# Kernel optimization log

Measured on AMD Instinct MI355X. Metric: run time of the kernel, lower is better.

The kernel has to match this reference:

```python
import jax, jax.numpy as jnp
import numpy as np

N_NODES = 50000
N_EDGES = 800000
D_IN = 128
D_OUT = 128


def setup_inputs() -> dict:
    key = jax.random.key(0)
    k1, k2, k3, k4, k5, k6 = jax.random.split(key, 6)
    x = jax.random.normal(k1, (N_NODES, D_IN), dtype=jnp.float32)
    edge_row = jnp.sort(jax.random.randint(k2, (N_EDGES,), 0, N_NODES, dtype=jnp.int32))
    edge_col = jax.random.randint(k3, (N_EDGES,), 0, N_NODES, dtype=jnp.int32)
    edge_val = jax.random.uniform(k4, (N_EDGES,), dtype=jnp.float32)
    W = jax.random.uniform(k5, (D_OUT, D_IN), dtype=jnp.float32)  # torch Linear weight [out,in], uniform_ init
    b = jax.random.normal(k6, (D_OUT,), dtype=jnp.float32)
    return {"x": x, "edge_row": edge_row, "edge_col": edge_col,
            "edge_val": edge_val, "W": W, "b": b}


def reference(x, edge_row, edge_col, edge_val, W, b):
    # spmm: out[i] = sum_{e: row[e]==i} val[e] * x[col[e]]
    msgs = x[edge_col] * edge_val[:, None]            # [E, D_IN]
    agg = jax.ops.segment_sum(msgs, edge_row, num_segments=x.shape[0])  # [N, D_IN]
    # dropout is identity in eval mode; linear projection y = agg @ W^T + b
    return agg @ W.T + b
```

## Files before the change

### kernel.cpp

```cpp
#include <hip/hip_runtime.h>
#include <hip/hip_bf16.h>


#define NPB     16
#define BLOCK   256
#define D       128
#define CHUNK   512
#define ASTRIDE 136

typedef __attribute__((ext_vector_type(8))) short bf16x8;
typedef __attribute__((ext_vector_type(4))) float f32x4;

__device__ __forceinline__ short f2bf(float f) {
    unsigned u = __float_as_uint(f);
    unsigned r = (u + 0x7fffu + ((u >> 16) & 1u)) >> 16;
    return (short)r;
}
__device__ __forceinline__ float bf_lo(int w) { return __int_as_float(w << 16); }
__device__ __forceinline__ float bf_hi(int w) { return __int_as_float(w & 0xffff0000); }

__global__ __launch_bounds__(256)
void prepass_kernel(const float* __restrict__ x,
                    const float* __restrict__ W,
                    const int*   __restrict__ edge_row,
                    short* __restrict__ xb,
                    short* __restrict__ wb,
                    int*   __restrict__ rs,
                    int n_nodes, int n_edges, int n4, int nw4)
{
    const int gid = blockIdx.x * 256 + threadIdx.x;

    if (gid <= n_nodes) {
        int lo = 0, hi = n_edges;
        while (lo < hi) {
            int mid = (lo + hi) >> 1;
            bool lt = (edge_row[mid] < gid);
            lo = lt ? (mid + 1) : lo;
            hi = lt ? hi : mid;
        }
        rs[gid] = lo;
    }

    const int i = gid - (n_nodes + 1);
    if (i >= 0 && i < n4) {
        float4 v = reinterpret_cast<const float4*>(x)[i];
        reinterpret_cast<short4*>(xb)[i] =
            make_short4(f2bf(v.x), f2bf(v.y), f2bf(v.z), f2bf(v.w));
    }

    const int iw = i - n4;
    if (iw >= 0 && iw < nw4) {
        float4 v = reinterpret_cast<const float4*>(W)[iw];
        reinterpret_cast<short4*>(wb)[iw] =
            make_short4(f2bf(v.x), f2bf(v.y), f2bf(v.z), f2bf(v.w));
    }
}

__global__ __launch_bounds__(BLOCK, 8)
void gcn_main_kernel(const short* __restrict__ xb,
                     const short* __restrict__ wb,
                     const int*   __restrict__ rs_g,
                     const int*   __restrict__ edge_col,
                     const float* __restrict__ edge_val,
                     const float* __restrict__ bvec,
                     float*       __restrict__ out,
                     int n_nodes, int n_edges)
{
    __shared__ int2  cv_s[CHUNK];
    __shared__ __align__(16) short agg_s[NPB * ASTRIDE];
    __shared__ int rs_s[NPB + 1];

    const int tid  = threadIdx.x;
    const int wave = tid >> 6;
    const int lane = tid & 63;
    const int tile_base = blockIdx.x * NPB;

    if (tid <= NPB) rs_s[tid] = rs_g[tile_base + tid];
    __syncthreads();

    const int E0 = __builtin_amdgcn_readfirstlane(rs_s[0]);
    const int E1 = __builtin_amdgcn_readfirstlane(rs_s[NPB]);

    const int p = lane >> 4;
    const int q = lane & 15;
    const int n = wave * 4 + p;
    const int e0 = rs_s[n], e1 = rs_s[n + 1];
    const short* xq = xb + q * 8;

    float2 acc2[4];
    #pragma unroll
    for (int i = 0; i < 4; ++i) acc2[i] = make_float2(0.f, 0.f);

    for (int cb = E0; cb < E1; cb += CHUNK) {
        const int cnt = min(E1 - cb, CHUNK);
        __syncthreads();
        for (int i = tid; i < cnt; i += BLOCK) {
            cv_s[i] = make_int2(edge_col[cb + i], __float_as_int(edge_val[cb + i]));
        }
        __syncthreads();

        const int s = max(e0, cb);
        const int t = min(e1, cb + cnt);
        int m = t - s;
        int mm = max(m, __shfl_xor(m, 16, 64));
        mm = max(mm, __shfl_xor(mm, 32, 64));
        mm = __builtin_amdgcn_readfirstlane(mm);

        for (int it = 0; it < mm; it += 8) {
            #pragma unroll
            for (int u = 0; u < 8; ++u) {
                int idx = s + it + u;
                bool ok = (idx < t);
                int il = ok ? (idx - cb) : 0;
                int2 cv = cv_s[il];
                float v = ok ? __int_as_float(cv.y) : 0.f;
                int4 xr = *reinterpret_cast<const int4*>(xq + ((size_t)cv.x << 7));
                float2 p0 = make_float2(bf_lo(xr.x), bf_hi(xr.x));
                float2 p1 = make_float2(bf_lo(xr.y), bf_hi(xr.y));
                float2 p2 = make_float2(bf_lo(xr.z), bf_hi(xr.z));
                float2 p3 = make_float2(bf_lo(xr.w), bf_hi(xr.w));
                acc2[0].x = fmaf(v, p0.x, acc2[0].x); acc2[0].y = fmaf(v, p0.y, acc2[0].y);
                acc2[1].x = fmaf(v, p1.x, acc2[1].x); acc2[1].y = fmaf(v, p1.y, acc2[1].y);
                acc2[2].x = fmaf(v, p2.x, acc2[2].x); acc2[2].y = fmaf(v, p2.y, acc2[2].y);
                acc2[3].x = fmaf(v, p3.x, acc2[3].x); acc2[3].y = fmaf(v, p3.y, acc2[3].y);
            }
        }
    }

    {
        bf16x8 o;
        o[0] = f2bf(acc2[0].x); o[1] = f2bf(acc2[0].y);
        o[2] = f2bf(acc2[1].x); o[3] = f2bf(acc2[1].y);
        o[4] = f2bf(acc2[2].x); o[5] = f2bf(acc2[2].y);
        o[6] = f2bf(acc2[3].x); o[7] = f2bf(acc2[3].y);
        *reinterpret_cast<bf16x8*>(&agg_s[n * ASTRIDE + q * 8]) = o;
    }

    const int n16 = lane & 15;
    const int g   = lane >> 4;

    bf16x8 bfr[2][4];
    float  bj[2];
    #pragma unroll
    for (int tt = 0; tt < 2; ++tt) {
        const int jt = 2 * wave + tt;
        const short* wrow = wb + ((size_t)(jt * 16 + n16)) * D + g * 8;
        #pragma unroll
        for (int ks = 0; ks < 4; ++ks) {
            bfr[tt][ks] = *reinterpret_cast<const bf16x8*>(wrow + ks * 32);
        }
        bj[tt] = bvec[jt * 16 + n16];
    }

    __syncthreads();

    {
        bf16x8 afr[4];
        #pragma unroll
        for (int ks = 0; ks < 4; ++ks) {
            afr[ks] = *reinterpret_cast<const bf16x8*>(
                &agg_s[n16 * ASTRIDE + ks * 32 + g * 8]);
        }

        #pragma unroll
        for (int tt = 0; tt < 2; ++tt) {
            const int jt = 2 * wave + tt;
            const int j  = jt * 16 + n16;

            f32x4 c = {0.f, 0.f, 0.f, 0.f};
            #pragma unroll
            for (int ks = 0; ks < 4; ++ks) {
                c = __builtin_amdgcn_mfma_f32_16x16x32_bf16(afr[ks], bfr[tt][ks], c, 0, 0, 0);
            }
            #pragma unroll
            for (int r = 0; r < 4; ++r) {
                int node = tile_base + g * 4 + r;
                if (node < n_nodes)
                    out[(size_t)node * D + j] = c[r] + bj[tt];
            }
        }
    }
}

__global__ __launch_bounds__(BLOCK, 5)
void gcn_fallback_kernel(const float* __restrict__ x,
                         const int*   __restrict__ edge_row,
                         const int*   __restrict__ edge_col,
                         const float* __restrict__ edge_val,
                         const float* __restrict__ W,
                         const float* __restrict__ bvec,
                         float*       __restrict__ out,
                         int n_nodes, int n_edges)
{
    __shared__ __align__(16) short agg_s[NPB * ASTRIDE];
    __shared__ int rs_s[NPB + 1];

    const int tid  = threadIdx.x;
    const int wave = tid >> 6;
    const int lane = tid & 63;
    const int tile_base = blockIdx.x * NPB;

    if (tid <= NPB) {
        int target = tile_base + tid;
        if (target > n_nodes) target = n_nodes;
        int lo = 0, hi = n_edges;
        while (lo < hi) {
            int mid = (lo + hi) >> 1;
            lo = (edge_row[mid] < target) ? (mid + 1) : lo;
            hi = (edge_row[mid] < target) ? hi : mid;
        }
        rs_s[tid] = lo;
    }
    __syncthreads();

    {
        const int h = lane >> 5;
        const int q = lane & 31;
        const float* xq = x + (q << 2);

        #pragma unroll
        for (int ni = 0; ni < NPB / 4; ++ni) {
            const int n = wave + 4 * ni;
            const int e0 = __builtin_amdgcn_readfirstlane(rs_s[n]);
            const int e1 = __builtin_amdgcn_readfirstlane(rs_s[n + 1]);
            float ax = 0.f, ay = 0.f, az = 0.f, aw = 0.f;
            for (int e = e0; e < e1; e += 16) {
                #pragma unroll
                for (int u = 0; u < 8; ++u) {
                    int idx  = e + 2 * u + h;
                    int idxc = (idx < e1) ? idx : (e1 - 1);
                    int   c  = edge_col[idxc];
                    float vr = edge_val[idxc];
                    float v  = (idx < e1) ? vr : 0.f;
                    float4 xr = *reinterpret_cast<const float4*>(xq + ((size_t)c << 7));
                    ax += v * xr.x; ay += v * xr.y; az += v * xr.z; aw += v * xr.w;
                }
            }
            ax += __shfl_xor(ax, 32, 64); ay += __shfl_xor(ay, 32, 64);
            az += __shfl_xor(az, 32, 64); aw += __shfl_xor(aw, 32, 64);
            if (h == 0) {
                *reinterpret_cast<short4*>(&agg_s[n * ASTRIDE + (q << 2)]) =
                    make_short4(f2bf(ax), f2bf(ay), f2bf(az), f2bf(aw));
            }
        }
    }

    const int n16 = lane & 15;
    const int g   = lane >> 4;
    bf16x8 bfr[2][4];
    #pragma unroll
    for (int tt = 0; tt < 2; ++tt) {
        const int jt = 2 * wave + tt;
        const float* rowp = W + ((size_t)(jt * 16 + n16)) * D + g * 8;
        #pragma unroll
        for (int ks = 0; ks < 4; ++ks) {
            float4 wa = *reinterpret_cast<const float4*>(rowp + ks * 32);
            float4 wb4 = *reinterpret_cast<const float4*>(rowp + ks * 32 + 4);
            bf16x8 f;
            f[0] = f2bf(wa.x); f[1] = f2bf(wa.y); f[2] = f2bf(wa.z); f[3] = f2bf(wa.w);
            f[4] = f2bf(wb4.x); f[5] = f2bf(wb4.y); f[6] = f2bf(wb4.z); f[7] = f2bf(wb4.w);
            bfr[tt][ks] = f;
        }
    }
    __syncthreads();
    {
        bf16x8 afr[4];
        #pragma unroll
        for (int ks = 0; ks < 4; ++ks)
            afr[ks] = *reinterpret_cast<const bf16x8*>(&agg_s[n16 * ASTRIDE + ks * 32 + g * 8]);
        #pragma unroll
        for (int tt = 0; tt < 2; ++tt) {
            const int jt = 2 * wave + tt;
            const int j  = jt * 16 + n16;
            const float bj = bvec[j];
            f32x4 c = {0.f, 0.f, 0.f, 0.f};
            #pragma unroll
            for (int ks = 0; ks < 4; ++ks)
                c = __builtin_amdgcn_mfma_f32_16x16x32_bf16(afr[ks], bfr[tt][ks], c, 0, 0, 0);
            #pragma unroll
            for (int r = 0; r < 4; ++r) {
                int node = tile_base + g * 4 + r;
                if (node < n_nodes)
                    out[(size_t)node * D + j] = c[r] + bj;
            }
        }
    }
}

extern "C" void kernel_launch(void* const* d_in, const int* in_sizes, int n_in,
                              void* d_out, int out_size, void* d_ws, size_t ws_size,
                              hipStream_t stream) {
    const float* x        = (const float*)d_in[0];
    const int*   edge_row = (const int*)  d_in[1];
    const int*   edge_col = (const int*)  d_in[2];
    const float* edge_val = (const float*)d_in[3];
    const float* W        = (const float*)d_in[4];
    const float* b        = (const float*)d_in[5];
    float* out = (float*)d_out;

    const int n_nodes = in_sizes[0] / D;
    const int n_edges = in_sizes[1];
    const int grid = (n_nodes + NPB - 1) / NPB;

    const size_t xb_bytes = (size_t)n_nodes * D * sizeof(short);
    const size_t rs_bytes = (size_t)(n_nodes + 1) * sizeof(int);
    const size_t wb_bytes = (size_t)D * D * sizeof(short);
    if (ws_size >= xb_bytes + rs_bytes + wb_bytes) {
        short* xb = (short*)d_ws;
        int*   rs = (int*)((char*)d_ws + xb_bytes);
        short* wb = (short*)((char*)d_ws + xb_bytes + rs_bytes);
        const int n4  = n_nodes * D / 4;
        const int nw4 = D * D / 4;
        const int total = (n_nodes + 1) + n4 + nw4;
        prepass_kernel<<<(total + 255) / 256, 256, 0, stream>>>(
            x, W, edge_row, xb, wb, rs, n_nodes, n_edges, n4, nw4);
        gcn_main_kernel<<<grid, BLOCK, 0, stream>>>(xb, wb, rs, edge_col, edge_val,
                                                    b, out, n_nodes, n_edges);
    } else {
        gcn_fallback_kernel<<<grid, BLOCK, 0, stream>>>(x, edge_row, edge_col, edge_val,
                                                        W, b, out, n_nodes, n_edges);
    }
}
```

Before: 127.9 us.

## Stage one edge chunk per block and batch gathers per node with global fallback

Replaces the per-chunk loop with its block-wide barriers by a single staging of up to one chunk of edges into shared memory. Each node group then walks only its own edges, issuing eight gathers before the FMAs so more loads are in flight; edges past the staged chunk are read straight from global memory. Accumulation uses packed two-float vectors, and the occupancy hint drops from 8 to 6 waves per SIMD to allow more registers for the batched loads. The risk is lower occupancy, plus a slow serial global path for the rare blocks with more edges than fit in one chunk.

```diff
diff --git a/kernel.cpp b/kernel.cpp
--- a/kernel.cpp
+++ b/kernel.cpp
@@ -10,6 +10,7 @@
 
 typedef __attribute__((ext_vector_type(8))) short bf16x8;
 typedef __attribute__((ext_vector_type(4))) float f32x4;
+typedef __attribute__((ext_vector_type(2))) float v2f;
 
 __device__ __forceinline__ short f2bf(float f) {
     unsigned u = __float_as_uint(f);
@@ -56,7 +57,7 @@
     }
 }
 
-__global__ __launch_bounds__(BLOCK, 8)
+__global__ __launch_bounds__(BLOCK, 6)
 void gcn_main_kernel(const short* __restrict__ xb,
                      const short* __restrict__ wb,
                      const int*   __restrict__ rs_g,
@@ -80,51 +81,57 @@
 
     const int E0 = __builtin_amdgcn_readfirstlane(rs_s[0]);
     const int E1 = __builtin_amdgcn_readfirstlane(rs_s[NPB]);
+    const int cnt = min(E1 - E0, CHUNK);
+
+    for (int i = tid; i < cnt; i += BLOCK) {
+        cv_s[i] = make_int2(edge_col[E0 + i], __float_as_int(edge_val[E0 + i]));
+    }
+    __syncthreads();
 
     const int p = lane >> 4;
     const int q = lane & 15;
     const int n = wave * 4 + p;
     const int e0 = rs_s[n], e1 = rs_s[n + 1];
+    const int cap  = E0 + cnt;
+    const int ecap = min(e1, cap);
     const short* xq = xb + q * 8;
 
-    float2 acc2[4];
+    v2f acc2[4];
     #pragma unroll
-    for (int i = 0; i < 4; ++i) acc2[i] = make_float2(0.f, 0.f);
-
-    for (int cb = E0; cb < E1; cb += CHUNK) {
-        const int cnt = min(E1 - cb, CHUNK);
-        __syncthreads();
-        for (int i = tid; i < cnt; i += BLOCK) {
-            cv_s[i] = make_int2(edge_col[cb + i], __float_as_int(edge_val[cb + i]));
-        }
-        __syncthreads();
-
-        const int s = max(e0, cb);
-        const int t = min(e1, cb + cnt);
-        int m = t - s;
-        int mm = max(m, __shfl_xor(m, 16, 64));
-        mm = max(mm, __shfl_xor(mm, 32, 64));
-        mm = __builtin_amdgcn_readfirstlane(mm);
-
-        for (int it = 0; it < mm; it += 8) {
-            #pragma unroll
-            for (int u = 0; u < 8; ++u) {
-                int idx = s + it + u;
-                bool ok = (idx < t);
-                int il = ok ? (idx - cb) : 0;
-                int2 cv = cv_s[il];
-                float v = ok ? __int_as_float(cv.y) : 0.f;
-                int4 xr = *reinterpret_cast<const int4*>(xq + ((size_t)cv.x << 7));
-                float2 p0 = make_float2(bf_lo(xr.x), bf_hi(xr.x));
-                float2 p1 = make_float2(bf_lo(xr.y), bf_hi(xr.y));
-                float2 p2 = make_float2(bf_lo(xr.z), bf_hi(xr.z));
-                float2 p3 = make_float2(bf_lo(xr.w), bf_hi(xr.w));
-                acc2[0].x = fmaf(v, p0.x, acc2[0].x); acc2[0].y = fmaf(v, p0.y, acc2[0].y);
-                acc2[1].x = fmaf(v, p1.x, acc2[1].x); acc2[1].y = fmaf(v, p1.y, acc2[1].y);
-                acc2[2].x = fmaf(v, p2.x, acc2[2].x); acc2[2].y = fmaf(v, p2.y, acc2[2].y);
-                acc2[3].x = fmaf(v, p3.x, acc2[3].x); acc2[3].y = fmaf(v, p3.y, acc2[3].y);
-            }
-        }
+    for (int i = 0; i < 4; ++i) acc2[i] = (v2f){0.f, 0.f};
+
+    for (int e = e0; e < ecap; e += 8) {
+        int2  cv[8];
+        int4  xr[8];
+        #pragma unroll
+        for (int u = 0; u < 8; ++u) {
+            int idx = e + u;
+            int il  = (idx < ecap) ? (idx - E0) : (e0 - E0);
+            cv[u] = cv_s[il];
+        }
+        #pragma unroll
+        for (int u = 0; u < 8; ++u) {
+            xr[u] = *reinterpret_cast<const int4*>(xq + ((size_t)cv[u].x << 7));
+        }
+        #pragma unroll
+        for (int u = 0; u < 8; ++u) {
+            float vm = (e + u < ecap) ? __int_as_float(cv[u].y) : 0.f;
+            v2f v2 = (v2f){vm, vm};
+            acc2[0] += v2 * (v2f){bf_lo(xr[u].x), bf_hi(xr[u].x)};
+            acc2[1] += v2 * (v2f){bf_lo(xr[u].y), bf_hi(xr[u].y)};
+            acc2[2] += v2 * (v2f){bf_lo(xr[u].z), bf_hi(xr[u].z)};
+            acc2[3] += v2 * (v2f){bf_lo(xr[u].w), bf_hi(xr[u].w)};
+        }
+    }
+    for (int e = max(e0, cap); e < e1; ++e) {
+        int   c = edge_col[e];
+        float v = edge_val[e];
+        int4 xr = *reinterpret_cast<const int4*>(xq + ((size_t)c << 7));
+        v2f v2 = (v2f){v, v};
+        acc2[0] += v2 * (v2f){bf_lo(xr.x), bf_hi(xr.x)};
+        acc2[1] += v2 * (v2f){bf_lo(xr.y), bf_hi(xr.y)};
+        acc2[2] += v2 * (v2f){bf_lo(xr.z), bf_hi(xr.z)};
+        acc2[3] += v2 * (v2f){bf_lo(xr.w), bf_hi(xr.w)};
     }
 
     {
@@ -254,10 +261,10 @@
         const float* rowp = W + ((size_t)(jt * 16 + n16)) * D + g * 8;
         #pragma unroll
         for (int ks = 0; ks < 4; ++ks) {
-            float4 wa = *reinterpret_cast<const float4*>(rowp + ks * 32);
+            float4 wa  = *reinterpret_cast<const float4*>(rowp + ks * 32);
             float4 wb4 = *reinterpret_cast<const float4*>(rowp + ks * 32 + 4);
             bf16x8 f;
-            f[0] = f2bf(wa.x); f[1] = f2bf(wa.y); f[2] = f2bf(wa.z); f[3] = f2bf(wa.w);
+            f[0] = f2bf(wa.x);  f[1] = f2bf(wa.y);  f[2] = f2bf(wa.z);  f[3] = f2bf(wa.w);
             f[4] = f2bf(wb4.x); f[5] = f2bf(wb4.y); f[6] = f2bf(wb4.z); f[7] = f2bf(wb4.w);
             bfr[tt][ks] = f;
         }
```

Result: faster. 122.4 us (-4.3%).
